# Performance work log

Hardware: AMD Instinct MI355X
Metric: run time of the kernel (lower is better)

The kernel has to match this reference:

```python
import jax, jax.numpy as jnp
import numpy as np

N = 50000
NEG_SLOPE = 0.2


def add_self_loops(edge_index, n):
    loops = jnp.arange(n, dtype=edge_index.dtype)
    return jnp.concatenate([edge_index, jnp.stack([loops, loops])], axis=1)


def gat_layer(x, edge_index, W, a_src, a_dst, b, heads, ch):
    # x: [N, F_in], W: [F_in, heads*ch], a_src/a_dst: [heads, ch], b: [heads*ch]
    n = x.shape[0]
    src, dst = edge_index[0], edge_index[1]
    h = (x @ W).reshape(n, heads, ch)                      # [N, H, C]
    alpha_src = jnp.sum(h * a_src, axis=-1)                # [N, H]
    alpha_dst = jnp.sum(h * a_dst, axis=-1)                # [N, H]
    e = jax.nn.leaky_relu(alpha_src[src] + alpha_dst[dst], NEG_SLOPE)  # [E, H]
    # segment softmax over incoming edges of each destination node
    m = jax.ops.segment_max(e, dst, num_segments=n)        # [N, H]
    ex = jnp.exp(e - m[dst])                               # [E, H]
    denom = jax.ops.segment_sum(ex, dst, num_segments=n)   # [N, H]
    alpha = ex / (denom[dst] + 1e-16)                      # [E, H]
    msg = h[src] * alpha[:, :, None]                       # [E, H, C]
    out = jax.ops.segment_sum(msg, dst, num_segments=n)    # [N, H, C]
    return out.reshape(n, heads * ch) + b


def setup_inputs() -> dict:
    key = jax.random.key(0)
    ks = jax.random.split(key, 12)
    input_dim, hidden_dim, output_dim, heads = 128, 32, 64, 4
    E = 1600000
    x = jax.random.normal(ks[0], (N, input_dim), dtype=jnp.float32)
    edge_index = jax.random.randint(ks[1], (2, E), 0, N, dtype=jnp.int64)
    s1 = 1.0 / np.sqrt(input_dim)
    s2 = 1.0 / np.sqrt(hidden_dim * heads)
    W1 = jax.random.uniform(ks[2], (input_dim, heads * hidden_dim), jnp.float32, -s1, s1)
    a_src1 = jax.random.uniform(ks[3], (heads, hidden_dim), jnp.float32, -s1, s1)
    a_dst1 = jax.random.uniform(ks[4], (heads, hidden_dim), jnp.float32, -s1, s1)
    b1 = jnp.zeros((heads * hidden_dim,), jnp.float32)
    W2 = jax.random.uniform(ks[5], (heads * hidden_dim, output_dim), jnp.float32, -s2, s2)
    a_src2 = jax.random.uniform(ks[6], (1, output_dim), jnp.float32, -s2, s2)
    a_dst2 = jax.random.uniform(ks[7], (1, output_dim), jnp.float32, -s2, s2)
    b2 = jnp.zeros((output_dim,), jnp.float32)
    return {"x": x, "edge_index": edge_index,
            "W1": W1, "a_src1": a_src1, "a_dst1": a_dst1, "b1": b1,
            "W2": W2, "a_src2": a_src2, "a_dst2": a_dst2, "b2": b2}


def reference(x, edge_index, W1, a_src1, a_dst1, b1, W2, a_src2, a_dst2, b2):
    n = x.shape[0]
    ei = add_self_loops(edge_index, n)
    h = gat_layer(x, ei, W1, a_src1, a_dst1, b1, heads=4, ch=32)
    h = jax.nn.relu(h)
    out = gat_layer(h, ei, W2, a_src2, a_dst2, b2, heads=1, ch=64)
    return out
```

## Files before the change

### kernel.cpp

```cpp
#include <hip/hip_runtime.h>
#include <hip/hip_bf16.h>
#include <hip/hip_fp16.h>


#define LRELU_SLOPE 0.2f
#define NBMAX 200
#define NBLK  512
#define BCAP  16384
#define CAPIMG 16384

__global__ __launch_bounds__(256) void hist_kernel(const int* __restrict__ ei_dst,
                                                   int* __restrict__ hist, int E, int chunk) {
    __shared__ int h[NBMAX];
    int t = threadIdx.x;
    for (int i = t; i < NBMAX; i += 256) h[i] = 0;
    __syncthreads();
    int begin = blockIdx.x * chunk;
    int endE = min(E, begin + chunk);
    for (int e = begin + t; e < endE; e += 256) atomicAdd(&h[ei_dst[e] >> 8], 1);
    __syncthreads();
    for (int i = t; i < NBMAX; i += 256) hist[i * NBLK + blockIdx.x] = h[i];
}

__global__ __launch_bounds__(512) void bucket_scan_kernel(int* __restrict__ hist,
                                                          int* __restrict__ gfill) {
    __shared__ int buf[2][NBLK];
    int b = blockIdx.x, t = threadIdx.x;
    buf[0][t] = hist[b * NBLK + t];
    __syncthreads();
    int pi = 0;
#pragma unroll
    for (int off = 1; off < NBLK; off <<= 1) {
        int v = buf[pi][t];
        if (t >= off) v += buf[pi][t - off];
        buf[pi ^ 1][t] = v;
        __syncthreads();
        pi ^= 1;
    }
    hist[b * NBLK + t] = (t == 0) ? 0 : buf[pi][t - 1];
    if (t == 0) gfill[b] = buf[pi][NBLK - 1];
}

__global__ __launch_bounds__(256) void scatter2_kernel(const int* __restrict__ ei_src,
                                                       const int* __restrict__ ei_dst,
                                                       const int* __restrict__ hist,
                                                       unsigned int* __restrict__ records,
                                                       int E, int chunk) {
    __shared__ int base[NBMAX];
    __shared__ int lcnt[NBMAX];
    int t = threadIdx.x;
    for (int i = t; i < NBMAX; i += 256) {
        base[i] = hist[i * NBLK + blockIdx.x];
        lcnt[i] = 0;
    }
    __syncthreads();
    int begin = blockIdx.x * chunk;
    int endE = min(E, begin + chunk);
    for (int e = begin + t; e < endE; e += 256) {
        int s = ei_src[e], d = ei_dst[e];
        int bkt = d >> 8;
        unsigned int rec = (unsigned int)d | ((unsigned int)s << 16);
        int r = atomicAdd(&lcnt[bkt], 1);
        records[(size_t)bkt * BCAP + base[bkt] + r] = rec;
    }
}

__global__ __launch_bounds__(256) void deg_kernel(const unsigned int* __restrict__ records,
                                                  const int* __restrict__ gfill,
                                                  int* __restrict__ deg, int N) {
    __shared__ int cnt[256];
    int t = threadIdx.x, b = blockIdx.x;
    cnt[t] = 1;
    __syncthreads();
    int c = gfill[b];
    const unsigned int* r = records + (size_t)b * BCAP;
    for (int i = t; i < c; i += 256) atomicAdd(&cnt[r[i] & 255], 1);
    __syncthreads();
    int gi = (b << 8) + t;
    if (gi < N) deg[gi] = cnt[t];
}

__global__ __launch_bounds__(256) void scan_blocksums_kernel(const int* __restrict__ gfill,
                                                             int* __restrict__ bsums,
                                                             int* __restrict__ row_ptr,
                                                             int nblocks, int n, int total) {
    __shared__ int buf[2][256];
    int t = threadIdx.x;
    int v0 = 0;
    if (t < nblocks) v0 = gfill[t] + min(256, n - (t << 8));
    buf[0][t] = v0;
    __syncthreads();
    int pi = 0;
#pragma unroll
    for (int off = 1; off < 256; off <<= 1) {
        int v = buf[pi][t];
        if (t >= off) v += buf[pi][t - off];
        buf[pi ^ 1][t] = v;
        __syncthreads();
        pi ^= 1;
    }
    if (t < nblocks) bsums[t] = (t == 0) ? 0 : buf[pi][t - 1];
    if (t == 0) row_ptr[n] = total;
}

__global__ __launch_bounds__(256) void scan_down_kernel(const int* __restrict__ deg,
                                                        const int* __restrict__ blockSums,
                                                        int* __restrict__ row_ptr, int n) {
    __shared__ int buf[2][256];
    int t = threadIdx.x;
    int i = blockIdx.x * 256 + t;
    int d = (i < n) ? deg[i] : 0;
    buf[0][t] = d;
    __syncthreads();
    int pi = 0;
#pragma unroll
    for (int off = 1; off < 256; off <<= 1) {
        int v = buf[pi][t];
        if (t >= off) v += buf[pi][t - off];
        buf[pi ^ 1][t] = v;
        __syncthreads();
        pi ^= 1;
    }
    if (i < n) row_ptr[i] = blockSums[blockIdx.x] + buf[pi][t] - d;
}

__global__ __launch_bounds__(256) void csr_scatter_kernel(const unsigned int* __restrict__ records,
                                                          const int* __restrict__ gfill,
                                                          const int* __restrict__ row_ptr,
                                                          unsigned short* __restrict__ col,
                                                          int N) {
    __shared__ unsigned short img[CAPIMG];
    __shared__ int lfill[256];
    int t = threadIdx.x, b = blockIdx.x;
    int bBase = b << 8;
    int bEnd = min(bBase + 256, N);
    int rbase = row_ptr[bBase];
    int size = row_ptr[bEnd] - rbase;
    bool lds = (size <= CAPIMG);
    int gi = bBase + t;
    if (gi < bEnd) {
        int rp = row_ptr[gi];
        int local = rp - rbase;
        lfill[t] = local + 1;
        if (lds) img[local] = (unsigned short)gi;
        else col[rp] = (unsigned short)gi;
    }
    __syncthreads();
    int c = gfill[b];
    const unsigned int* r = records + (size_t)b * BCAP;
    for (int i = t; i < c; i += 256) {
        unsigned int rec = r[i];
        int d8 = rec & 255;
        unsigned short s = (unsigned short)(rec >> 16);
        int p = atomicAdd(&lfill[d8], 1);
        if (lds) img[p] = s;
        else col[rbase + p] = s;
    }
    __syncthreads();
    if (lds) {
        for (int i = t; i < size; i += 256) col[rbase + i] = img[i];
    }
}


template <int M, int TN, int HEADS>
__global__ __launch_bounds__(256) void gemm_kernel(const float* __restrict__ X,
                                                   const float* __restrict__ W,
                                                   __half* __restrict__ outh,
                                                   const float* __restrict__ a_src,
                                                   const float* __restrict__ a_dst,
                                                   float* __restrict__ as_out,
                                                   float* __restrict__ ad_out, int nrows) {
    constexpr int KT = 32;
    constexpr int XS_STRIDE = 36;
    __shared__ float xs[64 * XS_STRIDE];
    __shared__ float ws[KT * M];
    int t = threadIdx.x;
    int tx = t & 15, ty = t >> 4;
    int rowBase = blockIdx.x * 64;

    float acc[4][TN];
#pragma unroll
    for (int r = 0; r < 4; ++r)
#pragma unroll
        for (int j = 0; j < TN; ++j) acc[r][j] = 0.f;

    for (int kt = 0; kt < 128; kt += KT) {
        {
            int rid = t >> 3;
            int c4 = (t & 7) * 4;
#pragma unroll
            for (int p = 0; p < 2; ++p) {
                int r = rid + 32 * p;
                int grow = rowBase + r;
                float4 v = make_float4(0.f, 0.f, 0.f, 0.f);
                if (grow < nrows) v = *(const float4*)(X + (size_t)grow * 128 + kt + c4);
                *(float4*)(xs + r * XS_STRIDE + c4) = v;
            }
        }
        {
            constexpr int NF = KT * M / 4;
            for (int f = t; f < NF; f += 256) {
                int kr = f / (M / 4);
                int c4w = (f % (M / 4)) * 4;
                *(float4*)(ws + kr * M + c4w) = *(const float4*)(W + (size_t)(kt + kr) * M + c4w);
            }
        }
        __syncthreads();
#pragma unroll
        for (int k = 0; k < KT; ++k) {
            float xr[4];
#pragma unroll
            for (int r = 0; r < 4; ++r) xr[r] = xs[(ty * 4 + r) * XS_STRIDE + k];
            float wv[TN];
#pragma unroll
            for (int j = 0; j < TN; ++j) wv[j] = ws[k * M + tx * TN + j];
#pragma unroll
            for (int r = 0; r < 4; ++r)
#pragma unroll
                for (int j = 0; j < TN; ++j) acc[r][j] = fmaf(xr[r], wv[j], acc[r][j]);
        }
        __syncthreads();
    }

    float aS[TN], aD[TN];
#pragma unroll
    for (int j = 0; j < TN; ++j) {
        aS[j] = a_src[tx * TN + j];
        aD[j] = a_dst[tx * TN + j];
    }
    constexpr int RW = (M / HEADS) / TN;
#pragma unroll
    for (int r = 0; r < 4; ++r) {
        int grow = rowBase + ty * 4 + r;
        float ss = 0.f, dd = 0.f;
#pragma unroll
        for (int j = 0; j < TN; ++j) {
            ss = fmaf(acc[r][j], aS[j], ss);
            dd = fmaf(acc[r][j], aD[j], dd);
        }
#pragma unroll
        for (int o = 1; o < RW; o <<= 1) {
            ss += __shfl_xor(ss, o, 64);
            dd += __shfl_xor(dd, o, 64);
        }
        if (grow < nrows) {
            if ((tx & (RW - 1)) == 0) {
                int head = tx / RW;
                as_out[grow * HEADS + head] = ss;
                ad_out[grow * HEADS + head] = dd;
            }
            alignas(16) __half tmp[TN];
#pragma unroll
            for (int j = 0; j < TN; ++j) tmp[j] = __float2half(acc[r][j]);
            if (TN == 8) {
                *(int4*)(outh + (size_t)grow * M + tx * TN) = *(int4*)tmp;
            } else {
                *(int2*)(outh + (size_t)grow * M + tx * TN) = *(int2*)tmp;
            }
        }
    }
}


__global__ __launch_bounds__(256) void agg1_kernel(const __half2* __restrict__ h1h,
                                                   const float* __restrict__ asrc,
                                                   const float* __restrict__ adst,
                                                   const int* __restrict__ row_ptr,
                                                   const unsigned short* __restrict__ col,
                                                   const float* __restrict__ b1,
                                                   float* __restrict__ out, int n) {
    int wave = threadIdx.x >> 6;
    int lane = threadIdx.x & 63;
    int node = blockIdx.x * 4 + wave;
    if (node >= n) return;
    int head = lane >> 4;
    int hp1 = lane & 3;
    int j16 = lane >> 2;
    float ad1 = adst[node * 4 + hp1];
    int start = row_ptr[node], end = row_ptr[node + 1];
    float accx = 0.f, accy = 0.f, s = 0.f;
    for (int base = start; base < end; base += 64) {
        int idx = base + lane;
        int cnt = min(64, end - base);
        int myS = (idx < end) ? (int)col[idx] : 0;
        float pr[4];
#pragma unroll
        for (int e = 0; e < 4; ++e) {
            int j = e * 16 + j16;
            int srcj = __shfl(myS, j, 64);
            float ev = asrc[srcj * 4 + hp1] + ad1;
            ev = (ev > 0.f) ? ev : LRELU_SLOPE * ev;
            pr[e] = (j < cnt) ? __expf(ev) : 0.f;
        }
#pragma unroll
        for (int e = 0; e < 4; ++e) {
            int ebase = e << 4;
            if (ebase < cnt) {
                float pre = pr[e];
                int rem4 = min(16, ((cnt - ebase) + 3) & ~3);
                for (int jj = 0; jj < rem4; jj += 4) {
                    int j0 = ebase + jj;
                    int s0 = __shfl(myS, j0, 64);
                    int s1 = __shfl(myS, j0 + 1, 64);
                    int s2 = __shfl(myS, j0 + 2, 64);
                    int s3 = __shfl(myS, j0 + 3, 64);
                    float p0 = __shfl(pre, (jj + 0) * 4 + head, 64);
                    float p1 = __shfl(pre, (jj + 1) * 4 + head, 64);
                    float p2 = __shfl(pre, (jj + 2) * 4 + head, 64);
                    float p3 = __shfl(pre, (jj + 3) * 4 + head, 64);
                    __half2 h0 = h1h[(size_t)s0 * 64 + lane];
                    __half2 h1v = h1h[(size_t)s1 * 64 + lane];
                    __half2 h2v = h1h[(size_t)s2 * 64 + lane];
                    __half2 h3v = h1h[(size_t)s3 * 64 + lane];
                    float2 f0 = __half22float2(h0);
                    float2 f1 = __half22float2(h1v);
                    float2 f2 = __half22float2(h2v);
                    float2 f3 = __half22float2(h3v);
                    accx = fmaf(p0, f0.x, accx);
                    accy = fmaf(p0, f0.y, accy);
                    accx = fmaf(p1, f1.x, accx);
                    accy = fmaf(p1, f1.y, accy);
                    accx = fmaf(p2, f2.x, accx);
                    accy = fmaf(p2, f2.y, accy);
                    accx = fmaf(p3, f3.x, accx);
                    accy = fmaf(p3, f3.y, accy);
                    s += (p0 + p1) + (p2 + p3);
                }
            }
        }
    }
    float inv = 1.f / (s + 1e-16f);
    float2 bb = ((const float2*)b1)[lane];
    float2 o;
    o.x = fmaxf(accx * inv + bb.x, 0.f);
    o.y = fmaxf(accy * inv + bb.y, 0.f);
    *(float2*)(out + (size_t)node * 128 + 2 * lane) = o;
}

__global__ __launch_bounds__(256) void agg2_kernel(const __half2* __restrict__ h2bh,
                                                   const float* __restrict__ asrc,
                                                   const float* __restrict__ adst,
                                                   const int* __restrict__ row_ptr,
                                                   const unsigned short* __restrict__ col,
                                                   const float* __restrict__ b2,
                                                   float* __restrict__ out, int n) {
    int wave = threadIdx.x >> 6;
    int lane = threadIdx.x & 63;
    int node = blockIdx.x * 4 + wave;
    if (node >= n) return;
    int half = lane >> 5;
    int m = lane & 31;
    float ad = adst[node];
    int start = row_ptr[node], end = row_ptr[node + 1];
    float accx = 0.f, accy = 0.f, s = 0.f;
    for (int base = start; base < end; base += 64) {
        int idx = base + lane;
        int cnt = min(64, end - base);
        int myS = (idx < end) ? (int)col[idx] : 0;
        float ev = asrc[myS] + ad;
        ev = (ev > 0.f) ? ev : LRELU_SLOPE * ev;
        float pr = (lane < cnt) ? __expf(ev) : 0.f;
        for (int j = 0; j < cnt; j += 8) {
            int j0 = j + half;
            int s0 = __shfl(myS, j0, 64);
            int s1 = __shfl(myS, j0 + 2, 64);
            int s2 = __shfl(myS, j0 + 4, 64);
            int s3 = __shfl(myS, j0 + 6, 64);
            float p0 = __shfl(pr, j0, 64);
            float p1 = __shfl(pr, j0 + 2, 64);
            float p2 = __shfl(pr, j0 + 4, 64);
            float p3 = __shfl(pr, j0 + 6, 64);
            __half2 h0 = h2bh[(size_t)s0 * 32 + m];
            __half2 h1v = h2bh[(size_t)s1 * 32 + m];
            __half2 h2v = h2bh[(size_t)s2 * 32 + m];
            __half2 h3v = h2bh[(size_t)s3 * 32 + m];
            float2 f0 = __half22float2(h0);
            float2 f1 = __half22float2(h1v);
            float2 f2 = __half22float2(h2v);
            float2 f3 = __half22float2(h3v);
            accx = fmaf(p0, f0.x, accx);
            accy = fmaf(p0, f0.y, accy);
            accx = fmaf(p1, f1.x, accx);
            accy = fmaf(p1, f1.y, accy);
            accx = fmaf(p2, f2.x, accx);
            accy = fmaf(p2, f2.y, accy);
            accx = fmaf(p3, f3.x, accx);
            accy = fmaf(p3, f3.y, accy);
            s += (p0 + p1) + (p2 + p3);
        }
    }
    s += __shfl_xor(s, 32, 64);
    accx += __shfl_xor(accx, 32, 64);
    accy += __shfl_xor(accy, 32, 64);
    if (half == 0) {
        float inv = 1.f / (s + 1e-16f);
        float2 bb = ((const float2*)b2)[m];
        float2 o;
        o.x = accx * inv + bb.x;
        o.y = accy * inv + bb.y;
        *(float2*)(out + (size_t)node * 64 + 2 * m) = o;
    }
}


extern "C" void kernel_launch(void* const* d_in, const int* in_sizes, int n_in,
                              void* d_out, int out_size, void* d_ws, size_t ws_size,
                              hipStream_t stream) {
    const float* x      = (const float*)d_in[0];
    const int*   ei     = (const int*)d_in[1];
    const float* W1     = (const float*)d_in[2];
    const float* a_src1 = (const float*)d_in[3];
    const float* a_dst1 = (const float*)d_in[4];
    const float* b1     = (const float*)d_in[5];
    const float* W2     = (const float*)d_in[6];
    const float* a_src2 = (const float*)d_in[7];
    const float* a_dst2 = (const float*)d_in[8];
    const float* b2     = (const float*)d_in[9];
    float* out = (float*)d_out;

    const int N = in_sizes[0] / 128;
    const int E = in_sizes[1] / 2;
    const int total = E + N;
    const int nBuckets = (N + 255) >> 8;

    char* ws = (char*)d_ws;
    size_t off = 0;
    auto alloc = [&](size_t bytes) {
        void* p = ws + off;
        off += (bytes + 255) & ~(size_t)255;
        return p;
    };
    float* regionA = (float*)alloc((size_t)N * 128 * 4);
    __half* h1h   = (__half*)alloc((size_t)N * 128 * 2);
    __half* h2bh  = (__half*)alloc((size_t)N * 64 * 2);
    float* asrc1  = (float*)alloc((size_t)N * 4 * 4);
    float* adst1  = (float*)alloc((size_t)N * 4 * 4);
    float* asrc2  = (float*)alloc((size_t)N * 4);
    float* adst2  = (float*)alloc((size_t)N * 4);
    int*   deg    = (int*)alloc((size_t)N * 4);
    int*   row_ptr= (int*)alloc((size_t)(N + 1) * 4);
    int*   gfill  = (int*)alloc((size_t)nBuckets * 4);
    int*   bsums  = (int*)alloc((size_t)nBuckets * 4);
    unsigned short* col = (unsigned short*)alloc((size_t)total * 2);

    unsigned int* records = (unsigned int*)regionA;
    int* hist = (int*)(regionA + (size_t)NBMAX * BCAP);
    float* h2in = regionA;
    (void)ws_size; (void)n_in; (void)out_size;

    const int* ei_src = ei;
    const int* ei_dst = ei + E;

    const int chunk = (E + NBLK - 1) / NBLK;
    hist_kernel<<<NBLK, 256, 0, stream>>>(ei_dst, hist, E, chunk);
    bucket_scan_kernel<<<nBuckets, NBLK, 0, stream>>>(hist, gfill);
    scatter2_kernel<<<NBLK, 256, 0, stream>>>(ei_src, ei_dst, hist, records, E, chunk);
    deg_kernel<<<nBuckets, 256, 0, stream>>>(records, gfill, deg, N);
    scan_blocksums_kernel<<<1, 256, 0, stream>>>(gfill, bsums, row_ptr, nBuckets, N, total);
    scan_down_kernel<<<nBuckets, 256, 0, stream>>>(deg, bsums, row_ptr, N);
    csr_scatter_kernel<<<nBuckets, 256, 0, stream>>>(records, gfill, row_ptr, col, N);

    gemm_kernel<128, 8, 4><<<(N + 63) / 64, 256, 0, stream>>>(x, W1, h1h, a_src1, a_dst1,
                                                              asrc1, adst1, N);
    agg1_kernel<<<(N + 3) / 4, 256, 0, stream>>>((const __half2*)h1h, asrc1, adst1,
                                                 row_ptr, col, b1, h2in, N);

    gemm_kernel<64, 4, 1><<<(N + 63) / 64, 256, 0, stream>>>(h2in, W2, h2bh, a_src2, a_dst2,
                                                             asrc2, adst2, N);
    agg2_kernel<<<(N + 3) / 4, 256, 0, stream>>>((const __half2*)h2bh, asrc2, adst2,
                                                 row_ptr, col, b2, out, N);
}
```

Measured before the change: 274.4 us.

## Use fp16 MFMA for both GEMMs and store layer-1 output as fp16

Both dense projections now run on 16x16x32 fp16 MFMA instructions instead of scalar FP32 FMAs, with W transposed into LDS as fp16 and the attention dot products reduced by cross-lane shuffles. The layer-1 aggregation output is written as half2, which halves its write traffic and the second GEMM's read traffic. The gather address arithmetic is also simplified to unsigned shift/or. This trades precision, since inputs to both GEMMs are rounded to fp16, for lower ALU and memory cost in the GEMM stages.

Measured after the change: 250.7 us. 1.09x faster.

```diff
diff --git a/kernel.cpp b/kernel.cpp
--- a/kernel.cpp
+++ b/kernel.cpp
@@ -8,6 +8,10 @@
 #define NBLK  512
 #define BCAP  16384
 #define CAPIMG 16384
+
+typedef _Float16 f16x8 __attribute__((ext_vector_type(8)));
+typedef float f32x4 __attribute__((ext_vector_type(4)));
+
 
 __global__ __launch_bounds__(256) void hist_kernel(const int* __restrict__ ei_dst,
                                                    int* __restrict__ hist, int E, int chunk) {
@@ -163,101 +167,156 @@
 }
 
 
-template <int M, int TN, int HEADS>
-__global__ __launch_bounds__(256) void gemm_kernel(const float* __restrict__ X,
-                                                   const float* __restrict__ W,
-                                                   __half* __restrict__ outh,
-                                                   const float* __restrict__ a_src,
-                                                   const float* __restrict__ a_dst,
-                                                   float* __restrict__ as_out,
-                                                   float* __restrict__ ad_out, int nrows) {
-    constexpr int KT = 32;
-    constexpr int XS_STRIDE = 36;
-    __shared__ float xs[64 * XS_STRIDE];
-    __shared__ float ws[KT * M];
+__global__ __launch_bounds__(256) void gemm1_mfma_kernel(const float* __restrict__ X,
+                                                         const float* __restrict__ W,
+                                                         __half* __restrict__ outh,
+                                                         const float* __restrict__ a_src,
+                                                         const float* __restrict__ a_dst,
+                                                         float* __restrict__ as_out,
+                                                         float* __restrict__ ad_out, int nrows) {
+    constexpr int KP = 136;
+    __shared__ _Float16 wlds[128 * KP];
     int t = threadIdx.x;
-    int tx = t & 15, ty = t >> 4;
-    int rowBase = blockIdx.x * 64;
-
-    float acc[4][TN];
-#pragma unroll
-    for (int r = 0; r < 4; ++r)
-#pragma unroll
-        for (int j = 0; j < TN; ++j) acc[r][j] = 0.f;
-
-    for (int kt = 0; kt < 128; kt += KT) {
-        {
-            int rid = t >> 3;
-            int c4 = (t & 7) * 4;
-#pragma unroll
-            for (int p = 0; p < 2; ++p) {
-                int r = rid + 32 * p;
-                int grow = rowBase + r;
-                float4 v = make_float4(0.f, 0.f, 0.f, 0.f);
-                if (grow < nrows) v = *(const float4*)(X + (size_t)grow * 128 + kt + c4);
-                *(float4*)(xs + r * XS_STRIDE + c4) = v;
+    int wv = t >> 6, lane = t & 63;
+    int quad = lane >> 4, m16 = lane & 15;
+    for (int i = t; i < 4096; i += 256) {
+        int k = i >> 5;
+        int n0 = (i & 31) << 2;
+        float4 v = *(const float4*)(W + k * 128 + n0);
+        wlds[(n0 + 0) * KP + k] = (_Float16)v.x;
+        wlds[(n0 + 1) * KP + k] = (_Float16)v.y;
+        wlds[(n0 + 2) * KP + k] = (_Float16)v.z;
+        wlds[(n0 + 3) * KP + k] = (_Float16)v.w;
+    }
+    __syncthreads();
+
+    int row = blockIdx.x * 64 + wv * 16 + m16;
+    int rowC = min(row, nrows - 1);
+    const float* xp = X + (size_t)rowC * 128;
+
+    f32x4 acc[8];
+#pragma unroll
+    for (int nt = 0; nt < 8; ++nt) acc[nt] = (f32x4)0.f;
+
+    for (int kt = 0; kt < 128; kt += 32) {
+        float4 v0 = *(const float4*)(xp + kt + quad * 8);
+        float4 v1 = *(const float4*)(xp + kt + quad * 8 + 4);
+        f16x8 af;
+        af[0] = (_Float16)v0.x; af[1] = (_Float16)v0.y;
+        af[2] = (_Float16)v0.z; af[3] = (_Float16)v0.w;
+        af[4] = (_Float16)v1.x; af[5] = (_Float16)v1.y;
+        af[6] = (_Float16)v1.z; af[7] = (_Float16)v1.w;
+#pragma unroll
+        for (int nt = 0; nt < 8; ++nt) {
+            f16x8 bf = *(const f16x8*)(&wlds[(nt * 16 + m16) * KP + kt + quad * 8]);
+            acc[nt] = __builtin_amdgcn_mfma_f32_16x16x32_f16(af, bf, acc[nt], 0, 0, 0);
+        }
+    }
+
+    float aS[8], aD[8];
+#pragma unroll
+    for (int nt = 0; nt < 8; ++nt) {
+        aS[nt] = a_src[nt * 16 + m16];
+        aD[nt] = a_dst[nt * 16 + m16];
+    }
+    int rowBaseW = blockIdx.x * 64 + wv * 16;
+#pragma unroll
+    for (int r = 0; r < 4; ++r) {
+        int orow = rowBaseW + quad * 4 + r;
+        bool ov = orow < nrows;
+        if (ov) {
+#pragma unroll
+            for (int nt = 0; nt < 8; ++nt)
+                outh[(size_t)orow * 128 + nt * 16 + m16] = __float2half(acc[nt][r]);
+        }
+#pragma unroll
+        for (int h = 0; h < 4; ++h) {
+            float ss = acc[2 * h][r] * aS[2 * h] + acc[2 * h + 1][r] * aS[2 * h + 1];
+            float dd = acc[2 * h][r] * aD[2 * h] + acc[2 * h + 1][r] * aD[2 * h + 1];
+#pragma unroll
+            for (int o = 1; o < 16; o <<= 1) {
+                ss += __shfl_xor(ss, o, 64);
+                dd += __shfl_xor(dd, o, 64);
             }
-        }
-        {
-            constexpr int NF = KT * M / 4;
-            for (int f = t; f < NF; f += 256) {
-                int kr = f / (M / 4);
-                int c4w = (f % (M / 4)) * 4;
-                *(float4*)(ws + kr * M + c4w) = *(const float4*)(W + (size_t)(kt + kr) * M + c4w);
+            if (ov && m16 == h) {
+                as_out[orow * 4 + h] = ss;
+                ad_out[orow * 4 + h] = dd;
             }
         }
-        __syncthreads();
-#pragma unroll
-        for (int k = 0; k < KT; ++k) {
-            float xr[4];
-#pragma unroll
-            for (int r = 0; r < 4; ++r) xr[r] = xs[(ty * 4 + r) * XS_STRIDE + k];
-            float wv[TN];
-#pragma unroll
-            for (int j = 0; j < TN; ++j) wv[j] = ws[k * M + tx * TN + j];
-#pragma unroll
-            for (int r = 0; r < 4; ++r)
-#pragma unroll
-                for (int j = 0; j < TN; ++j) acc[r][j] = fmaf(xr[r], wv[j], acc[r][j]);
-        }
-        __syncthreads();
-    }
-
-    float aS[TN], aD[TN];
-#pragma unroll
-    for (int j = 0; j < TN; ++j) {
-        aS[j] = a_src[tx * TN + j];
-        aD[j] = a_dst[tx * TN + j];
-    }
-    constexpr int RW = (M / HEADS) / TN;
+    }
+}
+
+
+__global__ __launch_bounds__(256) void gemm2_mfma_kernel(const __half* __restrict__ Xh,
+                                                         const float* __restrict__ W,
+                                                         __half* __restrict__ outh,
+                                                         const float* __restrict__ a_src,
+                                                         const float* __restrict__ a_dst,
+                                                         float* __restrict__ as_out,
+                                                         float* __restrict__ ad_out, int nrows) {
+    constexpr int KP = 136;
+    __shared__ _Float16 wlds[64 * KP];
+    int t = threadIdx.x;
+    int wv = t >> 6, lane = t & 63;
+    int quad = lane >> 4, m16 = lane & 15;
+    for (int i = t; i < 2048; i += 256) {
+        int k = i >> 4;
+        int n0 = (i & 15) << 2;
+        float4 v = *(const float4*)(W + k * 64 + n0);
+        wlds[(n0 + 0) * KP + k] = (_Float16)v.x;
+        wlds[(n0 + 1) * KP + k] = (_Float16)v.y;
+        wlds[(n0 + 2) * KP + k] = (_Float16)v.z;
+        wlds[(n0 + 3) * KP + k] = (_Float16)v.w;
+    }
+    __syncthreads();
+
+    int row = blockIdx.x * 64 + wv * 16 + m16;
+    int rowC = min(row, nrows - 1);
+    const _Float16* xp = (const _Float16*)Xh + (size_t)rowC * 128;
+
+    f32x4 acc[4];
+#pragma unroll
+    for (int nt = 0; nt < 4; ++nt) acc[nt] = (f32x4)0.f;
+
+    for (int kt = 0; kt < 128; kt += 32) {
+        f16x8 af = *(const f16x8*)(xp + kt + quad * 8);
+#pragma unroll
+        for (int nt = 0; nt < 4; ++nt) {
+            f16x8 bf = *(const f16x8*)(&wlds[(nt * 16 + m16) * KP + kt + quad * 8]);
+            acc[nt] = __builtin_amdgcn_mfma_f32_16x16x32_f16(af, bf, acc[nt], 0, 0, 0);
+        }
+    }
+
+    float aS[4], aD[4];
+#pragma unroll
+    for (int nt = 0; nt < 4; ++nt) {
+        aS[nt] = a_src[nt * 16 + m16];
+        aD[nt] = a_dst[nt * 16 + m16];
+    }
+    int rowBaseW = blockIdx.x * 64 + wv * 16;
 #pragma unroll
     for (int r = 0; r < 4; ++r) {
-        int grow = rowBase + ty * 4 + r;
+        int orow = rowBaseW + quad * 4 + r;
+        bool ov = orow < nrows;
+        if (ov) {
+#pragma unroll
+            for (int nt = 0; nt < 4; ++nt)
+                outh[(size_t)orow * 64 + nt * 16 + m16] = __float2half(acc[nt][r]);
+        }
         float ss = 0.f, dd = 0.f;
 #pragma unroll
-        for (int j = 0; j < TN; ++j) {
-            ss = fmaf(acc[r][j], aS[j], ss);
-            dd = fmaf(acc[r][j], aD[j], dd);
-        }
-#pragma unroll
-        for (int o = 1; o < RW; o <<= 1) {
+        for (int nt = 0; nt < 4; ++nt) {
+            ss = fmaf(acc[nt][r], aS[nt], ss);
+            dd = fmaf(acc[nt][r], aD[nt], dd);
+        }
+#pragma unroll
+        for (int o = 1; o < 16; o <<= 1) {
             ss += __shfl_xor(ss, o, 64);
             dd += __shfl_xor(dd, o, 64);
         }
-        if (grow < nrows) {
-            if ((tx & (RW - 1)) == 0) {
-                int head = tx / RW;
-                as_out[grow * HEADS + head] = ss;
-                ad_out[grow * HEADS + head] = dd;
-            }
-            alignas(16) __half tmp[TN];
-#pragma unroll
-            for (int j = 0; j < TN; ++j) tmp[j] = __float2half(acc[r][j]);
-            if (TN == 8) {
-                *(int4*)(outh + (size_t)grow * M + tx * TN) = *(int4*)tmp;
-            } else {
-                *(int2*)(outh + (size_t)grow * M + tx * TN) = *(int2*)tmp;
-            }
+        if (ov && m16 == 0) {
+            as_out[orow] = ss;
+            ad_out[orow] = dd;
         }
     }
 }
@@ -269,7 +328,7 @@
                                                    const int* __restrict__ row_ptr,
                                                    const unsigned short* __restrict__ col,
                                                    const float* __restrict__ b1,
-                                                   float* __restrict__ out, int n) {
+                                                   __half2* __restrict__ out, int n) {
     int wave = threadIdx.x >> 6;
     int lane = threadIdx.x & 63;
     int node = blockIdx.x * 4 + wave;
@@ -301,22 +360,18 @@
                 int rem4 = min(16, ((cnt - ebase) + 3) & ~3);
                 for (int jj = 0; jj < rem4; jj += 4) {
                     int j0 = ebase + jj;
-                    int s0 = __shfl(myS, j0, 64);
-                    int s1 = __shfl(myS, j0 + 1, 64);
-                    int s2 = __shfl(myS, j0 + 2, 64);
-                    int s3 = __shfl(myS, j0 + 3, 64);
+                    unsigned s0 = (unsigned)__shfl(myS, j0, 64);
+                    unsigned s1 = (unsigned)__shfl(myS, j0 + 1, 64);
+                    unsigned s2 = (unsigned)__shfl(myS, j0 + 2, 64);
+                    unsigned s3 = (unsigned)__shfl(myS, j0 + 3, 64);
                     float p0 = __shfl(pre, (jj + 0) * 4 + head, 64);
                     float p1 = __shfl(pre, (jj + 1) * 4 + head, 64);
                     float p2 = __shfl(pre, (jj + 2) * 4 + head, 64);
                     float p3 = __shfl(pre, (jj + 3) * 4 + head, 64);
-                    __half2 h0 = h1h[(size_t)s0 * 64 + lane];
-                    __half2 h1v = h1h[(size_t)s1 * 64 + lane];
-                    __half2 h2v = h1h[(size_t)s2 * 64 + lane];
-                    __half2 h3v = h1h[(size_t)s3 * 64 + lane];
-                    float2 f0 = __half22float2(h0);
-                    float2 f1 = __half22float2(h1v);
-                    float2 f2 = __half22float2(h2v);
-                    float2 f3 = __half22float2(h3v);
+                    float2 f0 = __half22float2(h1h[(s0 << 6) | lane]);
+                    float2 f1 = __half22float2(h1h[(s1 << 6) | lane]);
+                    float2 f2 = __half22float2(h1h[(s2 << 6) | lane]);
+                    float2 f3 = __half22float2(h1h[(s3 << 6) | lane]);
                     accx = fmaf(p0, f0.x, accx);
                     accy = fmaf(p0, f0.y, accy);
                     accx = fmaf(p1, f1.x, accx);
@@ -332,10 +387,9 @@
     }
     float inv = 1.f / (s + 1e-16f);
     float2 bb = ((const float2*)b1)[lane];
-    float2 o;
-    o.x = fmaxf(accx * inv + bb.x, 0.f);
-    o.y = fmaxf(accy * inv + bb.y, 0.f);
-    *(float2*)(out + (size_t)node * 128 + 2 * lane) = o;
+    float ox = fmaxf(accx * inv + bb.x, 0.f);
+    float oy = fmaxf(accy * inv + bb.y, 0.f);
+    out[((unsigned)node << 6) | lane] = __floats2half2_rn(ox, oy);
 }
 
 __global__ __launch_bounds__(256) void agg2_kernel(const __half2* __restrict__ h2bh,
@@ -363,22 +417,18 @@
         float pr = (lane < cnt) ? __expf(ev) : 0.f;
         for (int j = 0; j < cnt; j += 8) {
             int j0 = j + half;
-            int s0 = __shfl(myS, j0, 64);
-            int s1 = __shfl(myS, j0 + 2, 64);
-            int s2 = __shfl(myS, j0 + 4, 64);
-            int s3 = __shfl(myS, j0 + 6, 64);
+            unsigned s0 = (unsigned)__shfl(myS, j0, 64);
+            unsigned s1 = (unsigned)__shfl(myS, j0 + 2, 64);
+            unsigned s2 = (unsigned)__shfl(myS, j0 + 4, 64);
+            unsigned s3 = (unsigned)__shfl(myS, j0 + 6, 64);
             float p0 = __shfl(pr, j0, 64);
             float p1 = __shfl(pr, j0 + 2, 64);
             float p2 = __shfl(pr, j0 + 4, 64);
             float p3 = __shfl(pr, j0 + 6, 64);
-            __half2 h0 = h2bh[(size_t)s0 * 32 + m];
-            __half2 h1v = h2bh[(size_t)s1 * 32 + m];
-            __half2 h2v = h2bh[(size_t)s2 * 32 + m];
-            __half2 h3v = h2bh[(size_t)s3 * 32 + m];
-            float2 f0 = __half22float2(h0);
-            float2 f1 = __half22float2(h1v);
-            float2 f2 = __half22float2(h2v);
-            float2 f3 = __half22float2(h3v);
+            float2 f0 = __half22float2(h2bh[(s0 << 5) | m]);
+            float2 f1 = __half22float2(h2bh[(s1 << 5) | m]);
+            float2 f2 = __half22float2(h2bh[(s2 << 5) | m]);
+            float2 f3 = __half22float2(h2bh[(s3 << 5) | m]);
             accx = fmaf(p0, f0.x, accx);
             accy = fmaf(p0, f0.y, accy);
             accx = fmaf(p1, f1.x, accx);
@@ -446,7 +496,7 @@
 
     unsigned int* records = (unsigned int*)regionA;
     int* hist = (int*)(regionA + (size_t)NBMAX * BCAP);
-    float* h2in = regionA;
+    __half* h2in = (__half*)regionA;
     (void)ws_size; (void)n_in; (void)out_size;
 
     const int* ei_src = ei;
@@ -461,13 +511,13 @@
     scan_down_kernel<<<nBuckets, 256, 0, stream>>>(deg, bsums, row_ptr, N);
     csr_scatter_kernel<<<nBuckets, 256, 0, stream>>>(records, gfill, row_ptr, col, N);
 
-    gemm_kernel<128, 8, 4><<<(N + 63) / 64, 256, 0, stream>>>(x, W1, h1h, a_src1, a_dst1,
-                                                              asrc1, adst1, N);
+    gemm1_mfma_kernel<<<(N + 63) / 64, 256, 0, stream>>>(x, W1, h1h, a_src1, a_dst1,
+                                                         asrc1, adst1, N);
     agg1_kernel<<<(N + 3) / 4, 256, 0, stream>>>((const __half2*)h1h, asrc1, adst1,
-                                                 row_ptr, col, b1, h2in, N);
-
-    gemm_kernel<64, 4, 1><<<(N + 63) / 64, 256, 0, stream>>>(h2in, W2, h2bh, a_src2, a_dst2,
-                                                             asrc2, adst2, N);
+                                                 row_ptr, col, b1, (__half2*)h2in, N);
+
+    gemm2_mfma_kernel<<<(N + 63) / 64, 256, 0, stream>>>(h2in, W2, h2bh, a_src2, a_dst2,
+                                                         asrc2, adst2, N);
     agg2_kernel<<<(N + 3) / 4, 256, 0, stream>>>((const __half2*)h2bh, asrc2, adst2,
                                                  row_ptr, col, b2, out, N);
 }
```
